# Performance work log

Measured on AMD Instinct MI355X. Metric: run time of the kernel, lower is better.

Reference implementation:

```python
import jax, jax.numpy as jnp
import numpy as np

TH_SIM_MIN = 0.9
TH_DIFF_MAX = 0.1
BIG = 1e9
EPS = 1e-8


def setup_inputs() -> dict:
    key = jax.random.key(0)
    k1, k2 = jax.random.split(key)
    B, T, D = 16, 2048, 128
    embeddings = jax.random.normal(k1, (B, T, D), dtype=jnp.float32)
    label = jax.random.randint(k2, (B, T), 0, 2, dtype=jnp.int32)
    return {"embeddings": embeddings, "label": label}


def _masked_mean(vals, row_mask):
    # mean of vals over rows where row_mask is True; 0-safe denominator
    cnt = jnp.sum(row_mask, axis=-1).astype(vals.dtype)
    s = jnp.sum(jnp.where(row_mask, vals, 0.0), axis=-1)
    return s / jnp.maximum(cnt, 1.0)


def reference(embeddings, label):
    B = embeddings.shape[0]
    # pairwise cosine similarity per batch: [B, T, T]
    w = jnp.linalg.norm(embeddings, axis=-1, keepdims=True)  # [B,T,1]
    sim = jnp.einsum('bid,bjd->bij', embeddings, embeddings)
    sim = sim / jnp.maximum(w * jnp.swapaxes(w, 1, 2), EPS)

    fake = (label == 0)  # [B,T]
    real = (label == 1)
    fake_col = fake[:, None, :]
    real_col = real[:, None, :]

    # f2f: for each fake i, min over fake j (diagonal included, as in torch)
    f2f_min = jnp.min(jnp.where(fake_col, sim, BIG), axis=2)
    loss_f2f = _masked_mean(jnp.maximum(TH_SIM_MIN - f2f_min, 0.0), fake)

    # r2r: for each real i, min over real j
    r2r_min = jnp.min(jnp.where(real_col, sim, BIG), axis=2)
    loss_r2r = _masked_mean(jnp.maximum(TH_SIM_MIN - r2r_min, 0.0), real)

    # f2r: for each fake i, max over real j
    f2r_max = jnp.max(jnp.where(real_col, sim, -BIG), axis=2)
    loss_f2r = _masked_mean(jnp.maximum(f2r_max - TH_DIFF_MAX, 0.0), fake)

    # r2f: for each real i, max over fake j
    r2f_max = jnp.max(jnp.where(fake_col, sim, -BIG), axis=2)
    loss_r2f = _masked_mean(jnp.maximum(r2f_max - TH_DIFF_MAX, 0.0), real)

    # torch code `continue`s (adds nothing) when either class is empty
    valid = (jnp.sum(fake, axis=1) > 0) & (jnp.sum(real, axis=1) > 0)
    per_batch = jnp.where(valid, loss_f2f + loss_r2r + loss_f2r + loss_r2f, 0.0)
    return jnp.sum(per_batch) / B
```

## Files before the change

kernel.cpp:

```cpp
#include <hip/hip_runtime.h>
#include <hip/hip_bf16.h>

typedef __bf16 bf16x8 __attribute__((ext_vector_type(8)));
typedef float  f32x4  __attribute__((ext_vector_type(4)));

namespace {
constexpr int kB = 16;
constexpr int kT = 2048;
constexpr int kD = 128;
constexpr int RB = 64;
constexpr int CT = 64;
constexpr int NT = kT / CT;
constexpr float TH_SIM  = 0.9f;
constexpr float TH_DIFF = 0.1f;
constexpr float BIGF    = 1e9f;
}

static __device__ __forceinline__ void gload_lds16(const short* g, short* l) {
    __builtin_amdgcn_global_load_lds(
        (const __attribute__((address_space(1))) void*)g,
        (__attribute__((address_space(3))) void*)l, 16, 0, 0);
}

__global__ __launch_bounds__(256) void scan_kernel(const int* __restrict__ label,
                                                   int* __restrict__ perm,
                                                   int* __restrict__ cFarr) {
    const int b = blockIdx.x, tid = threadIdx.x;
    const int* lb = label + b * kT;
    int loc[8], cnt = 0;
    #pragma unroll
    for (int j = 0; j < 8; ++j) { loc[j] = (lb[tid * 8 + j] == 0); cnt += loc[j]; }
    __shared__ int s[256];
    s[tid] = cnt;
    __syncthreads();
    for (int off = 1; off < 256; off <<= 1) {
        const int v = (tid >= off) ? s[tid - off] : 0;
        __syncthreads();
        s[tid] += v;
        __syncthreads();
    }
    const int total = s[255];
    if (tid == 0) cFarr[b] = total;
    int run = s[tid] - cnt;
    #pragma unroll
    for (int j = 0; j < 8; ++j) {
        const int i = tid * 8 + j;
        perm[b * kT + i] = loc[j] ? run : (total + i - run);
        run += loc[j];
    }
}

__global__ __launch_bounds__(256) void nrm_kernel(const float* __restrict__ emb,
                                                  const int* __restrict__ perm,
                                                  __hip_bfloat16* __restrict__ out) {
    const int wave = threadIdx.x >> 6;
    const int lane = threadIdx.x & 63;
    const int row  = blockIdx.x * 4 + wave;
    const float2 v = *reinterpret_cast<const float2*>(emb + (size_t)row * kD + lane * 2);
    float ss = v.x * v.x + v.y * v.y;
    #pragma unroll
    for (int m = 1; m < 64; m <<= 1) ss += __shfl_xor(ss, m);
    const float inv = ss > 0.f ? rsqrtf(ss) : 0.f;
    const int b   = row >> 11;
    const int dst = perm[row];
    __hip_bfloat162 o;
    o.x = __float2bfloat16(v.x * inv);
    o.y = __float2bfloat16(v.y * inv);
    *reinterpret_cast<__hip_bfloat162*>(out + ((size_t)(b * kT + dst)) * kD + lane * 2) = o;
}

template <int MODE>
__device__ __forceinline__ void compute_tile(const short* __restrict__ buf,
                                             const bf16x8 (&afrag)[4][4],
                                             float (&u1)[4][4], float (&u2)[4][4],
                                             int col, int hi, int cGlob, int cf) {
    bf16x8 bfrag[4];
    #pragma unroll
    for (int kk = 0; kk < 4; ++kk) {
        const int sh = (kk * 32 + hi * 8) ^ ((col & 7) << 3);
        bfrag[kk] = *reinterpret_cast<const bf16x8*>(&buf[col * kD + sh]);
    }
    const bool cfake = (MODE == 2) && (cGlob < cf);
    #pragma unroll
    for (int rg = 0; rg < 4; ++rg) {
        f32x4 acc = {0.f, 0.f, 0.f, 0.f};
        #pragma unroll
        for (int kk = 0; kk < 4; ++kk)
            acc = __builtin_amdgcn_mfma_f32_16x16x32_bf16(afrag[rg][kk], bfrag[kk], acc, 0, 0, 0);
        if (MODE == 0) {
            #pragma unroll
            for (int r = 0; r < 4; ++r) u1[rg][r] = fminf(u1[rg][r], acc[r]);
        } else if (MODE == 1) {
            #pragma unroll
            for (int r = 0; r < 4; ++r) u2[rg][r] = fminf(u2[rg][r], -acc[r]);
        } else {
            #pragma unroll
            for (int r = 0; r < 4; ++r) {
                u1[rg][r] = fminf(u1[rg][r], cfake ? acc[r] : BIGF);
                u2[rg][r] = fminf(u2[rg][r], cfake ? BIGF : -acc[r]);
            }
        }
    }
}

__global__ __launch_bounds__(256, 2) void crloss_main(const __hip_bfloat16* __restrict__ nrm,
                                                      const int* __restrict__ cFarr,
                                                      float* __restrict__ partials) {
    __shared__ __align__(16) short lds[2][CT * kD];
    __shared__ float mrg[2][4][RB];
    const int bid  = blockIdx.x;
    const int b    = bid >> 5;
    const int rb   = bid & 31;
    const int tid  = threadIdx.x;
    const int wave = tid >> 6;
    const int lane = tid & 63;
    const int lo   = lane & 15;
    const int hi   = lane >> 4;

    const short* nb = reinterpret_cast<const short*>(nrm) + (size_t)b * kT * kD;
    const int cf   = cFarr[b];
    const int row0 = rb * RB;
    const int col  = wave * 16 + lo;

    bf16x8 afrag[4][4];
    #pragma unroll
    for (int rg = 0; rg < 4; ++rg) {
        #pragma unroll
        for (int kk = 0; kk < 4; ++kk)
            afrag[rg][kk] = *reinterpret_cast<const bf16x8*>(
                nb + (size_t)(row0 + rg * 16 + lo) * kD + kk * 32 + hi * 8);
        if (row0 + rg * 16 + lo >= cf) {
            unsigned* u = reinterpret_cast<unsigned*>(&afrag[rg][0]);
            #pragma unroll
            for (int q = 0; q < 16; ++q) u[q] ^= 0x80008000u;
        }
    }

    float u1[4][4], u2[4][4];
    #pragma unroll
    for (int rg = 0; rg < 4; ++rg)
        #pragma unroll
        for (int r = 0; r < 4; ++r) { u1[rg][r] = BIGF; u2[rg][r] = BIGF; }

    auto stage = [&](int ct, int bufIdx) {
        #pragma unroll
        for (int p = 0; p < 4; ++p) {
            const int unit = p * 4 + wave;
            const int c    = unit * 64 + lane;
            const int scol = c >> 4;
            const int sh   = ((c & 15) * 8) ^ ((scol & 7) << 3);
            gload_lds16(nb + (size_t)(ct * CT + scol) * kD + sh,
                        &lds[bufIdx][unit * 512]);
        }
    };

    const int  ctF    = cf >> 6;
    const bool hasMix = (cf & 63) != 0;

    stage(0, 0);
    __syncthreads();
    int cur = 0;
    for (int ct = 0; ct < NT; ++ct) {
        if (ct + 1 < NT) stage(ct + 1, cur ^ 1);
        if (ct < ctF)
            compute_tile<0>(lds[cur], afrag, u1, u2, col, hi, ct * CT + col, cf);
        else if (ct == ctF && hasMix)
            compute_tile<2>(lds[cur], afrag, u1, u2, col, hi, ct * CT + col, cf);
        else
            compute_tile<1>(lds[cur], afrag, u1, u2, col, hi, ct * CT + col, cf);
        __syncthreads();
        cur ^= 1;
    }

    #pragma unroll
    for (int m = 1; m <= 8; m <<= 1) {
        #pragma unroll
        for (int rg = 0; rg < 4; ++rg)
            #pragma unroll
            for (int r = 0; r < 4; ++r) {
                u1[rg][r] = fminf(u1[rg][r], __shfl_xor(u1[rg][r], m));
                u2[rg][r] = fminf(u2[rg][r], __shfl_xor(u2[rg][r], m));
            }
    }

    if (lo == 0) {
        #pragma unroll
        for (int rg = 0; rg < 4; ++rg)
            #pragma unroll
            for (int r = 0; r < 4; ++r) {
                mrg[0][wave][rg * 16 + hi * 4 + r] = u1[rg][r];
                mrg[1][wave][rg * 16 + hi * 4 + r] = u2[rg][r];
            }
    }
    __syncthreads();
    if (tid < RB) {
        const int row = tid;
        float a1 = BIGF, a2 = BIGF;
        #pragma unroll
        for (int w = 0; w < 4; ++w) {
            a1 = fminf(a1, mrg[0][w][row]);
            a2 = fminf(a2, mrg[1][w][row]);
        }
        const bool f   = (row0 + row) < cf;
        const float mn = f ? a1 : a2;
        const float mx = f ? -a2 : -a1;
        const float l  = fmaxf(TH_SIM - mn, 0.f) + fmaxf(mx - TH_DIFF, 0.f);
        float sF = f ? l : 0.f;
        float sR = f ? 0.f : l;
        #pragma unroll
        for (int m = 1; m < 64; m <<= 1) {
            sF += __shfl_xor(sF, m);
            sR += __shfl_xor(sR, m);
        }
        if (tid == 0) {
            partials[bid * 2]     = sF;
            partials[bid * 2 + 1] = sR;
        }
    }
}

__global__ __launch_bounds__(512) void crloss_final(const float* __restrict__ partials,
                                                    const int* __restrict__ cFarr,
                                                    float* __restrict__ out) {
    const int t = threadIdx.x;
    float pf = partials[t * 2];
    float pr = partials[t * 2 + 1];
    #pragma unroll
    for (int m = 1; m <= 16; m <<= 1) {
        pf += __shfl_xor(pf, m);
        pr += __shfl_xor(pr, m);
    }
    __shared__ float sF[16], sR[16];
    if ((t & 31) == 0) { sF[t >> 5] = pf; sR[t >> 5] = pr; }
    __syncthreads();
    if (t == 0) {
        float tot = 0.f;
        for (int b = 0; b < kB; ++b) {
            const int cf = cFarr[b], cr = kT - cf;
            if (cf > 0 && cr > 0)
                tot += sF[b] / (float)cf + sR[b] / (float)cr;
        }
        out[0] = tot / (float)kB;
    }
}

extern "C" void kernel_launch(void* const* d_in, const int* in_sizes, int n_in,
                              void* d_out, int out_size, void* d_ws, size_t ws_size,
                              hipStream_t stream) {
    const float* emb   = (const float*)d_in[0];
    const int*   label = (const int*)d_in[1];
    float*       out   = (float*)d_out;

    char* ws = (char*)d_ws;
    __hip_bfloat16* nrm = (__hip_bfloat16*)ws;
    int*   perm     = (int*)(ws + (size_t)kB * kT * kD * 2);
    int*   cFarr    = (int*)(ws + (size_t)kB * kT * kD * 2 + kB * kT * 4);
    float* partials = (float*)(ws + (size_t)kB * kT * kD * 2 + kB * kT * 4 + 64);

    scan_kernel<<<kB, 256, 0, stream>>>(label, perm, cFarr);
    nrm_kernel<<<kB * kT / 4, 256, 0, stream>>>(emb, perm, nrm);
    crloss_main<<<kB * (kT / RB), 256, 0, stream>>>(nrm, cFarr, partials);
    crloss_final<<<1, 512, 0, stream>>>(partials, cFarr, out);
}
```

Measured before the change: 56.55 us.

## Load B fragments directly from global into registers, drop LDS staging

The main loop no longer stages column tiles through double-buffered LDS with global_load_lds and barriers. Each lane now loads its own B fragments straight from global memory into a two-deep register double buffer, software-pipelined across tiles. This removes the LDS round trip and the per-tile __syncthreads. In exchange it adds register pressure, and global reads are no longer shared through LDS, so the same data is fetched once per wave instead of once per block, relying on L2 and L1 cache hits.

Result: no change. 57.66 us (+2.0%).

```diff
diff --git a/kernel.cpp b/kernel.cpp
--- a/kernel.cpp
+++ b/kernel.cpp
@@ -16,12 +16,6 @@
 constexpr float BIGF    = 1e9f;
 }
 
-static __device__ __forceinline__ void gload_lds16(const short* g, short* l) {
-    __builtin_amdgcn_global_load_lds(
-        (const __attribute__((address_space(1))) void*)g,
-        (__attribute__((address_space(3))) void*)l, 16, 0, 0);
-}
-
 __global__ __launch_bounds__(256) void scan_kernel(const int* __restrict__ label,
                                                    int* __restrict__ perm,
                                                    int* __restrict__ cFarr) {
@@ -70,17 +64,10 @@
 }
 
 template <int MODE>
-__device__ __forceinline__ void compute_tile(const short* __restrict__ buf,
+__device__ __forceinline__ void compute_vals(const bf16x8 (&bfrag)[4],
                                              const bf16x8 (&afrag)[4][4],
                                              float (&u1)[4][4], float (&u2)[4][4],
-                                             int col, int hi, int cGlob, int cf) {
-    bf16x8 bfrag[4];
-    #pragma unroll
-    for (int kk = 0; kk < 4; ++kk) {
-        const int sh = (kk * 32 + hi * 8) ^ ((col & 7) << 3);
-        bfrag[kk] = *reinterpret_cast<const bf16x8*>(&buf[col * kD + sh]);
-    }
-    const bool cfake = (MODE == 2) && (cGlob < cf);
+                                             bool cfake) {
     #pragma unroll
     for (int rg = 0; rg < 4; ++rg) {
         f32x4 acc = {0.f, 0.f, 0.f, 0.f};
@@ -106,7 +93,6 @@
 __global__ __launch_bounds__(256, 2) void crloss_main(const __hip_bfloat16* __restrict__ nrm,
                                                       const int* __restrict__ cFarr,
                                                       float* __restrict__ partials) {
-    __shared__ __align__(16) short lds[2][CT * kD];
     __shared__ float mrg[2][4][RB];
     const int bid  = blockIdx.x;
     const int b    = bid >> 5;
@@ -142,34 +128,33 @@
         #pragma unroll
         for (int r = 0; r < 4; ++r) { u1[rg][r] = BIGF; u2[rg][r] = BIGF; }
 
-    auto stage = [&](int ct, int bufIdx) {
-        #pragma unroll
-        for (int p = 0; p < 4; ++p) {
-            const int unit = p * 4 + wave;
-            const int c    = unit * 64 + lane;
-            const int scol = c >> 4;
-            const int sh   = ((c & 15) * 8) ^ ((scol & 7) << 3);
-            gload_lds16(nb + (size_t)(ct * CT + scol) * kD + sh,
-                        &lds[bufIdx][unit * 512]);
-        }
+    const short* bp = nb + (size_t)col * kD + hi * 8;
+    auto loadB = [&](bf16x8 (&bf)[4], int ct) {
+        const short* p = bp + (size_t)ct * (CT * kD);
+        #pragma unroll
+        for (int kk = 0; kk < 4; ++kk)
+            bf[kk] = *reinterpret_cast<const bf16x8*>(p + kk * 32);
     };
 
     const int  ctF    = cf >> 6;
     const bool hasMix = (cf & 63) != 0;
-
-    stage(0, 0);
-    __syncthreads();
-    int cur = 0;
-    for (int ct = 0; ct < NT; ++ct) {
-        if (ct + 1 < NT) stage(ct + 1, cur ^ 1);
+    auto comp = [&](const bf16x8 (&bf)[4], int ct) {
         if (ct < ctF)
-            compute_tile<0>(lds[cur], afrag, u1, u2, col, hi, ct * CT + col, cf);
+            compute_vals<0>(bf, afrag, u1, u2, false);
         else if (ct == ctF && hasMix)
-            compute_tile<2>(lds[cur], afrag, u1, u2, col, hi, ct * CT + col, cf);
+            compute_vals<2>(bf, afrag, u1, u2, (ct * CT + col) < cf);
         else
-            compute_tile<1>(lds[cur], afrag, u1, u2, col, hi, ct * CT + col, cf);
-        __syncthreads();
-        cur ^= 1;
+            compute_vals<1>(bf, afrag, u1, u2, false);
+    };
+
+    bf16x8 bA[4], bB[4];
+    loadB(bA, 0);
+    loadB(bB, 1);
+    for (int ct = 0; ct < NT; ct += 2) {
+        comp(bA, ct);
+        if (ct + 2 < NT) loadB(bA, ct + 2);
+        comp(bB, ct + 1);
+        if (ct + 3 < NT) loadB(bB, ct + 3);
     }
 
     #pragma unroll
```
